# Optimization experiments

Measured on AMD Instinct MI355X. Metric: run time of the kernel, lower is better.

## Reference

```python
import jax, jax.numpy as jnp
import numpy as np

D = 1024   # model dim (hard-coded in ClsNet)
H = 16     # num_heads
HD = D // H
FF = 2048  # torch TransformerEncoderLayer default dim_feedforward
B, LX, LY = 8, 512, 512
EPS = 1e-5
NEG = -1e9


def setup_inputs() -> dict:
    key = jax.random.key(0)
    ks = jax.random.split(key, 16)
    s = 0.02
    inp = {
        "x": jax.random.normal(ks[0], (B, LX, D), jnp.float32),
        "y": jax.random.normal(ks[1], (B, LY, D), jnp.float32),
        "cls": jax.random.normal(ks[2], (D,), jnp.float32) * s,
        "sep": jax.random.normal(ks[3], (D,), jnp.float32) * s,
        "px": jax.random.normal(ks[4], (D,), jnp.float32) * s,
        "py": jax.random.normal(ks[5], (D,), jnp.float32) * s,
        "Wqkv": jax.random.normal(ks[6], (3 * D, D), jnp.float32) * s,
        "bqkv": jnp.zeros((3 * D,), jnp.float32),
        "Wo": jax.random.normal(ks[7], (D, D), jnp.float32) * s,
        "bo": jnp.zeros((D,), jnp.float32),
        "W1": jax.random.normal(ks[8], (FF, D), jnp.float32) * s,
        "b1": jnp.zeros((FF,), jnp.float32),
        "W2": jax.random.normal(ks[9], (D, FF), jnp.float32) * s,
        "b2": jnp.zeros((D,), jnp.float32),
        "ln1_g": jnp.ones((D,), jnp.float32),
        "ln1_b": jnp.zeros((D,), jnp.float32),
        "ln2_g": jnp.ones((D,), jnp.float32),
        "ln2_b": jnp.zeros((D,), jnp.float32),
        "x_len": jax.random.randint(ks[10], (B,), 1, LX + 1, jnp.int32),
        "y_len": jax.random.randint(ks[11], (B,), 1, LY + 1, jnp.int32),
    }
    return inp


def _merge(x, y, cls, sep, px, py, x_len, y_len):
    # Vectorized version of ClsNet.merge: [CLS] x_i+px ... [SEP] y_i+py ... [SEP] pad...
    Bn, Lx, Dd = x.shape
    Ly = y.shape[1]
    S = Lx + Ly + 3
    pos = jnp.arange(S)[None, :]            # [1,S]
    lx = x_len[:, None]                     # [B,1]
    ly = y_len[:, None]
    is_cls = pos == 0                       # [1,S]
    is_x = (pos >= 1) & (pos <= lx)         # [B,S]
    is_sep1 = pos == lx + 1
    is_y = (pos >= lx + 2) & (pos <= lx + ly + 1)
    is_sep2 = pos == lx + ly + 2
    xi = jnp.clip(pos - 1, 0, Lx - 1)       # [1,S]
    yi = jnp.clip(pos - lx - 2, 0, Ly - 1)  # [B,S]
    xg = jnp.take_along_axis(x, xi[:, :, None], axis=1)  # [B,S,D] (broadcast batch)
    yg = jnp.take_along_axis(y, yi[:, :, None], axis=1)  # [B,S,D]
    seq = (jnp.where(is_x[..., None], xg + px, 0.0)
           + jnp.where(is_y[..., None], yg + py, 0.0)
           + is_cls[..., None] * cls
           + (is_sep1 | is_sep2)[..., None] * sep)       # [B,S,D]
    mask = is_cls | is_x | is_sep1 | is_y | is_sep2      # [B,S] True = valid token
    return seq, mask


def _ln(h, g, b):
    m = jnp.mean(h, axis=-1, keepdims=True)
    v = jnp.mean(jnp.square(h - m), axis=-1, keepdims=True)
    return (h - m) * jax.lax.rsqrt(v + EPS) * g + b


def _encoder_layer(seq, mask, Wqkv, bqkv, Wo, bo, W1, b1, W2, b2, ln1_g, ln1_b, ln2_g, ln2_b):
    Bn, S, Dd = seq.shape
    qkv = seq @ Wqkv.T + bqkv                              # [B,S,3D]
    q, k, v = jnp.split(qkv, 3, axis=-1)
    q = q.reshape(Bn, S, H, HD)
    k = k.reshape(Bn, S, H, HD)
    v = v.reshape(Bn, S, H, HD)
    bias = jnp.where(mask, 0.0, NEG)[:, None, None, :]     # padded KEYS masked out
    scores = jnp.einsum("bqhd,bkhd->bhqk", q, k) / np.sqrt(HD) + bias
    attn = jax.nn.softmax(scores, axis=-1)
    o = jnp.einsum("bhqk,bkhd->bqhd", attn, v).reshape(Bn, S, Dd)
    o = o @ Wo.T + bo
    h = _ln(seq + o, ln1_g, ln1_b)                          # post-norm (torch default)
    f = jax.nn.relu(h @ W1.T + b1) @ W2.T + b2
    return _ln(h + f, ln2_g, ln2_b)


def reference(x, y, cls, sep, px, py, Wqkv, bqkv, Wo, bo, W1, b1, W2, b2,
              ln1_g, ln1_b, ln2_g, ln2_b, x_len, y_len):
    seq, mask = _merge(x, y, cls, sep, px, py, x_len, y_len)
    out = _encoder_layer(seq, mask, Wqkv, bqkv, Wo, bo, W1, b1, W2, b2,
                         ln1_g, ln1_b, ln2_g, ln2_b)
    # torch code returns a[0] of the seq-first tensor -> the CLS position for all batches
    return out[:, 0, :]
```

## Files before the change

### kernel.cpp

```cpp
#include <hip/hip_runtime.h>
#include <hip/hip_bf16.h>

#define D_ 1024
#define H_ 16
#define FF_ 2048
#define B_ 8
#define S_ 1027
#define MPAD_ 8320
#define PSTR_ 1056
#define EPS_ 1e-5f

typedef __hip_bfloat16 bf16;
typedef unsigned short u16;
typedef unsigned int u32;
typedef __attribute__((ext_vector_type(4))) float floatx4;
typedef __bf16 bf16x8 __attribute__((ext_vector_type(8)));

__device__ __forceinline__ float2 bfpair(u32 u) {
  union { u32 u; float f; } lo, hi;
  lo.u = u << 16; hi.u = u & 0xffff0000u;
  return make_float2(lo.f, hi.f);
}

__device__ __forceinline__ u32 f2bfbits(float f) {
  union { bf16 h; u16 u; } cv; cv.h = __float2bfloat16(f); return (u32)cv.u;
}

__device__ __forceinline__ float block_sum(float x, float* red) {
  const int t = threadIdx.x;
  __syncthreads();
  red[t] = x;
  __syncthreads();
  for (int s = 128; s > 0; s >>= 1) {
    if (t < s) red[t] += red[t + s];
    __syncthreads();
  }
  return red[0];
}

__device__ __forceinline__ float block_max(float x, float* red) {
  const int t = threadIdx.x;
  __syncthreads();
  red[t] = x;
  __syncthreads();
  for (int s = 128; s > 0; s >>= 1) {
    if (t < s) red[t] = fmaxf(red[t], red[t + s]);
    __syncthreads();
  }
  return red[0];
}

__global__ void __launch_bounds__(256) build_seq_kernel(
    const float* __restrict__ x, const float* __restrict__ y,
    const float* __restrict__ cls, const float* __restrict__ sep,
    const float* __restrict__ px, const float* __restrict__ py,
    const int* __restrict__ x_len, const int* __restrict__ y_len,
    bf16* __restrict__ seq) {
  const int m = blockIdx.x, t = threadIdx.x;
  const int b = m / S_;
  const int s = m - b * S_;
  if (b >= B_) return;
  const float* src = nullptr;
  const float* add = nullptr;
  const int lx = x_len[b], ly = y_len[b];
  if (s == 0) src = cls;
  else if (s <= lx) { src = x + ((size_t)b * 512 + (s - 1)) * D_; add = px; }
  else if (s == lx + 1) src = sep;
  else if (s <= lx + ly + 1) { src = y + ((size_t)b * 512 + (s - lx - 2)) * D_; add = py; }
  else if (s == lx + ly + 2) src = sep;
  if (!src) return;
  float4 sv = ((const float4*)src)[t];
  if (add) {
    float4 av = ((const float4*)add)[t];
    sv.x += av.x; sv.y += av.y; sv.z += av.z; sv.w += av.w;
  }
  uint2 o;
  o.x = f2bfbits(sv.x) | (f2bfbits(sv.y) << 16);
  o.y = f2bfbits(sv.z) | (f2bfbits(sv.w) << 16);
  ((uint2*)(seq + (size_t)m * D_))[t] = o;
}

__global__ void __launch_bounds__(256) qproj_kernel(
    const float* __restrict__ cls, const float* __restrict__ Wqkv,
    const float* __restrict__ bqkv, float* __restrict__ q0s) {
  __shared__ float cl[D_];
  const int t = threadIdx.x;
  *(float4*)&cl[t * 4] = ((const float4*)cls)[t];
  __syncthreads();
  const int w = t >> 6, l = t & 63;
  const int r = blockIdx.x * 4 + w;
  float acc = 0.f;
#pragma unroll
  for (int ch = 0; ch < 4; ++ch) {
    float4 wv = *(const float4*)(Wqkv + (size_t)r * D_ + ch * 256 + l * 4);
    const float* c4 = &cl[ch * 256 + l * 4];
    acc += wv.x * c4[0] + wv.y * c4[1] + wv.z * c4[2] + wv.w * c4[3];
  }
#pragma unroll
  for (int off = 32; off > 0; off >>= 1) acc += __shfl_down(acc, off, 64);
  if (l == 0) q0s[r] = (acc + bqkv[r]) * 0.125f;
}

__global__ void __launch_bounds__(256) rproj_kernel(
    const float* __restrict__ Wqkv, const float* __restrict__ q0s,
    u16* __restrict__ RT_hi, u16* __restrict__ RT_lo) {
  const int h = blockIdx.y, cc = blockIdx.x, t = threadIdx.x;
  __shared__ float qs[64];
  if (t < 64) qs[t] = q0s[h * 64 + t];
  __syncthreads();
  const int c = cc * 256 + t;
  const float* Wk = Wqkv + (size_t)(D_ + h * 64) * D_ + c;
  float acc = 0.f;
#pragma unroll 8
  for (int e = 0; e < 64; ++e) acc += Wk[(size_t)e * D_] * qs[e];
  const u32 hb = f2bfbits(acc);
  union { u32 u; float f; } hv; hv.u = hb << 16;
  RT_hi[h * D_ + c] = (u16)hb;
  RT_lo[h * D_ + c] = (u16)f2bfbits(acc - hv.f);
}

__global__ void __launch_bounds__(256) scores_kernel(
    const bf16* __restrict__ seq, const u16* __restrict__ RT_hi,
    const u16* __restrict__ RT_lo, const int* __restrict__ x_len,
    const int* __restrict__ y_len, float* __restrict__ S) {
  const int m0 = blockIdx.x * 64;
  bool valid = false;
#pragma unroll
  for (int b = 0; b < B_; ++b) {
    int rs = b * S_, re = rs + x_len[b] + y_len[b] + 3;
    if (m0 < re && m0 + 64 > rs) valid = true;
  }
  if (!valid) return;
  const int t = threadIdx.x;
  const int w = t >> 6, lane = t & 63, lane16 = lane & 15, quad = lane >> 4;
  const int row = m0 + w * 16 + lane16;
  const u16* arow = (const u16*)seq + (size_t)row * D_ + quad * 8;
  const u16* bh = RT_hi + lane16 * D_ + quad * 8;
  const u16* bl = RT_lo + lane16 * D_ + quad * 8;
  floatx4 acc = {};
#pragma unroll 4
  for (int kt = 0; kt < 32; ++kt) {
    bf16x8 a  = *(const bf16x8*)(arow + kt * 32);
    bf16x8 vh = *(const bf16x8*)(bh + kt * 32);
    bf16x8 vl = *(const bf16x8*)(bl + kt * 32);
    acc = __builtin_amdgcn_mfma_f32_16x16x32_bf16(a, vh, acc, 0, 0, 0);
    acc = __builtin_amdgcn_mfma_f32_16x16x32_bf16(a, vl, acc, 0, 0, 0);
  }
  *(floatx4*)&S[(size_t)lane16 * MPAD_ + m0 + w * 16 + quad * 4] = acc;
}

__global__ void __launch_bounds__(256) softmax_kernel(
    const float* __restrict__ S, const int* __restrict__ x_len,
    const int* __restrict__ y_len, u16* __restrict__ P) {
  const int h = blockIdx.x, b = blockIdx.y, t = threadIdx.x;
  const int n = x_len[b] + y_len[b] + 3;
  __shared__ float sc[PSTR_];
  __shared__ float red[256];
  const float* Sp = S + (size_t)h * MPAD_ + b * S_;
  float lmax = -3.0e38f;
  for (int k = t; k < n; k += 256) {
    float s = Sp[k];
    sc[k] = s;
    lmax = fmaxf(lmax, s);
  }
  const float gmax = block_max(lmax, red);
  float lsum = 0.f;
  for (int k = t; k < n; k += 256) {
    float p = __expf(sc[k] - gmax);
    sc[k] = p;
    lsum += p;
  }
  const float inv = 1.0f / block_sum(lsum, red);
  u16* Pp = P + (size_t)(h * 8 + b) * PSTR_;
  for (int k = t; k < PSTR_; k += 256)
    Pp[k] = (k < n) ? (u16)f2bfbits(sc[k] * inv) : (u16)0;
}

__global__ void __launch_bounds__(256) cbar_kernel(
    const bf16* __restrict__ seq, const u16* __restrict__ P,
    const int* __restrict__ x_len, const int* __restrict__ y_len,
    float* __restrict__ cbar) {
  const int ct = blockIdx.x, b = blockIdx.y, t = threadIdx.x;
  const int c0 = ct * 64;
  const int n = x_len[b] + y_len[b] + 3;
  const int nkt = (n + 31) >> 5;
  __shared__ u16 tile[32 * 68];
  const int w = t >> 6, lane = t & 63, lane16 = lane & 15, quad = lane >> 4;
  const int sk = t >> 3, scg = (t & 7) * 8;
  floatx4 acc = {};
  for (int kt = 0; kt < nkt; ++kt) {
    const int k0 = kt * 32;
    __syncthreads();
    uint4 v = make_uint4(0u, 0u, 0u, 0u);
    if (k0 + sk < n)
      v = *(const uint4*)((const u16*)seq + (size_t)(b * S_ + k0 + sk) * D_ + c0 + scg);
    *(uint2*)&tile[sk * 68 + scg]     = make_uint2(v.x, v.y);
    *(uint2*)&tile[sk * 68 + scg + 4] = make_uint2(v.z, v.w);
    __syncthreads();
    bf16x8 a = *(const bf16x8*)(P + (size_t)(lane16 * 8 + b) * PSTR_ + k0 + quad * 8);
    union { bf16x8 v; u16 u[8]; } bu;
#pragma unroll
    for (int j = 0; j < 8; ++j)
      bu.u[j] = tile[(quad * 8 + j) * 68 + w * 16 + lane16];
    acc = __builtin_amdgcn_mfma_f32_16x16x32_bf16(a, bu.v, acc, 0, 0, 0);
  }
#pragma unroll
  for (int r = 0; r < 4; ++r)
    cbar[(size_t)(b * 16 + quad * 4 + r) * D_ + c0 + w * 16 + lane16] = acc[r];
}

template <int K, int N, int BSTR, bool INBF, bool OUTBF, bool RELU, bool PERHEAD>
__global__ void __launch_bounds__(256) gemv8_kernel(
    const void* __restrict__ in_, const float* __restrict__ W,
    const float* __restrict__ bias, void* __restrict__ out_) {
  const int t = threadIdx.x;
  const int hoff = PERHEAD ? ((blockIdx.x * 4) >> 6) * D_ : 0;
  __shared__ u16 lsb[INBF ? 8 * K : 1];
  __shared__ float lsf[INBF ? 1 : 8 * K];
  if (INBF) {
    const u16* in = (const u16*)in_;
    const int per = 8 * K / (256 * 8);
#pragma unroll
    for (int i = 0; i < per; ++i) {
      int flat = (t + i * 256) * 8;
      int b = flat / K, k = flat % K;
      *(uint4*)&lsb[flat] = *(const uint4*)(in + (size_t)b * BSTR + hoff + k);
    }
  } else {
    const float* in = (const float*)in_;
    const int per = 8 * K / (256 * 4);
#pragma unroll
    for (int i = 0; i < per; ++i) {
      int flat = (t + i * 256) * 4;
      int b = flat / K, k = flat % K;
      *(float4*)&lsf[flat] = *(const float4*)(in + (size_t)b * BSTR + hoff + k);
    }
  }
  __syncthreads();
  const int w = t >> 6, l = t & 63;
  const int r = blockIdx.x * 4 + w;
  float acc[8] = {};
#pragma unroll
  for (int ch = 0; ch < K / 256; ++ch) {
    float4 wv = *(const float4*)(W + (size_t)r * K + ch * 256 + l * 4);
#pragma unroll
    for (int b = 0; b < 8; ++b) {
      float i0, i1, i2, i3;
      if (INBF) {
        uint2 u = *(const uint2*)&lsb[b * K + ch * 256 + l * 4];
        float2 p0 = bfpair(u.x), p1 = bfpair(u.y);
        i0 = p0.x; i1 = p0.y; i2 = p1.x; i3 = p1.y;
      } else {
        const float* p = &lsf[b * K + ch * 256 + l * 4];
        i0 = p[0]; i1 = p[1]; i2 = p[2]; i3 = p[3];
      }
      acc[b] += wv.x * i0 + wv.y * i1 + wv.z * i2 + wv.w * i3;
    }
  }
#pragma unroll
  for (int off = 32; off > 0; off >>= 1)
#pragma unroll
    for (int b = 0; b < 8; ++b) acc[b] += __shfl_down(acc[b], off, 64);
  if (l == 0) {
    const float bs = bias[r];
#pragma unroll
    for (int b = 0; b < 8; ++b) {
      float v = acc[b] + bs;
      if (RELU) v = fmaxf(v, 0.f);
      if (OUTBF) ((bf16*)out_)[(size_t)b * N + r] = __float2bfloat16(v);
      else       ((float*)out_)[(size_t)b * N + r] = v;
    }
  }
}

template <bool SECOND>
__global__ void __launch_bounds__(256) ln_kernel(
    const float* __restrict__ cls, const float* __restrict__ a,
    const float* __restrict__ bvec, const float* __restrict__ g,
    const float* __restrict__ be, float* __restrict__ out) {
  const int b = blockIdx.x, t = threadIdx.x;
  __shared__ float v[D_];
  __shared__ float red[256];
  for (int i = t; i < D_; i += 256) {
    float val;
    if (SECOND) val = a[b * D_ + i] + bvec[b * D_ + i];
    else        val = cls[i] + a[b * D_ + i];
    v[i] = val;
  }
  __syncthreads();
  float ls = 0.f;
  for (int i = t; i < D_; i += 256) ls += v[i];
  const float mean = block_sum(ls, red) * (1.f / D_);
  float lv = 0.f;
  for (int i = t; i < D_; i += 256) { float dk = v[i] - mean; lv += dk * dk; }
  const float var = block_sum(lv, red) * (1.f / D_);
  const float rs = rsqrtf(var + EPS_);
  for (int i = t; i < D_; i += 256)
    out[b * D_ + i] = (v[i] - mean) * rs * g[i] + be[i];
}

extern "C" void kernel_launch(void* const* d_in, const int* in_sizes, int n_in,
                              void* d_out, int out_size, void* d_ws, size_t ws_size,
                              hipStream_t stream) {
  (void)in_sizes; (void)n_in; (void)out_size; (void)ws_size;
  const float* x    = (const float*)d_in[0];
  const float* y    = (const float*)d_in[1];
  const float* cls  = (const float*)d_in[2];
  const float* sep  = (const float*)d_in[3];
  const float* px   = (const float*)d_in[4];
  const float* py   = (const float*)d_in[5];
  const float* Wqkv = (const float*)d_in[6];
  const float* bqkv = (const float*)d_in[7];
  const float* Wo   = (const float*)d_in[8];
  const float* bo   = (const float*)d_in[9];
  const float* W1   = (const float*)d_in[10];
  const float* b1   = (const float*)d_in[11];
  const float* W2   = (const float*)d_in[12];
  const float* b2   = (const float*)d_in[13];
  const float* g1   = (const float*)d_in[14];
  const float* be1  = (const float*)d_in[15];
  const float* g2   = (const float*)d_in[16];
  const float* be2  = (const float*)d_in[17];
  const int* xl     = (const int*)d_in[18];
  const int* yl     = (const int*)d_in[19];

  char* ws = (char*)d_ws;
  bf16*  seq   = (bf16*)(ws);
  float* q0s   = (float*)(ws + 17039360);
  u16*   RT_hi = (u16*)(ws + 17043456);
  u16*   RT_lo = (u16*)(ws + 17076224);
  float* S     = (float*)(ws + 17108992);
  u16*   P     = (u16*)(ws + 17641472);
  float* cbar  = (float*)(ws + 17911808);
  float* o0    = (float*)(ws + 18436096);
  float* att   = (float*)(ws + 18468864);
  float* h0    = (float*)(ws + 18501632);
  bf16*  f1    = (bf16*)(ws + 18534400);
  float* f2    = (float*)(ws + 18567168);

  build_seq_kernel<<<MPAD_, 256, 0, stream>>>(x, y, cls, sep, px, py, xl, yl, seq);
  qproj_kernel<<<256, 256, 0, stream>>>(cls, Wqkv, bqkv, q0s);
  rproj_kernel<<<dim3(4, 16), 256, 0, stream>>>(Wqkv, q0s, RT_hi, RT_lo);
  scores_kernel<<<130, 256, 0, stream>>>(seq, RT_hi, RT_lo, xl, yl, S);
  softmax_kernel<<<dim3(16, 8), 256, 0, stream>>>(S, xl, yl, P);
  cbar_kernel<<<dim3(16, 8), 256, 0, stream>>>(seq, P, xl, yl, cbar);
  gemv8_kernel<1024, 1024, 16384, false, false, false, true>
      <<<256, 256, 0, stream>>>(cbar, Wqkv + (size_t)2048 * 1024, bqkv + 2048, o0);
  gemv8_kernel<1024, 1024, 1024, false, false, false, false>
      <<<256, 256, 0, stream>>>(o0, Wo, bo, att);
  ln_kernel<false><<<B_, 256, 0, stream>>>(cls, att, nullptr, g1, be1, h0);
  gemv8_kernel<1024, 2048, 1024, false, true, true, false>
      <<<512, 256, 0, stream>>>(h0, W1, b1, f1);
  gemv8_kernel<2048, 1024, 2048, true, false, false, false>
      <<<256, 256, 0, stream>>>(f1, W2, b2, f2);
  ln_kernel<true><<<B_, 256, 0, stream>>>(nullptr, h0, f2, g2, be2, (float*)d_out);
}
```

Before: 195.3 us.

## Fuse the whole pipeline into one cooperative persistent kernel with grid syncs

```diff
diff --git a/kernel.cpp b/kernel.cpp
--- a/kernel.cpp
+++ b/kernel.cpp
@@ -1,14 +1,21 @@
 #include <hip/hip_runtime.h>
 #include <hip/hip_bf16.h>
+#include <hip/hip_cooperative_groups.h>
+
+namespace cg = cooperative_groups;
 
 #define D_ 1024
 #define H_ 16
 #define FF_ 2048
 #define B_ 8
 #define S_ 1027
+#define BS_ 8216
 #define MPAD_ 8320
 #define PSTR_ 1056
 #define EPS_ 1e-5f
+#define MAXGRID_ 512
+#define NTILE_ 130
+#define SPLIT_KT_ 17
 
 typedef __hip_bfloat16 bf16;
 typedef unsigned short u16;
@@ -24,6 +31,376 @@
 
 __device__ __forceinline__ u32 f2bfbits(float f) {
   union { bf16 h; u16 u; } cv; cv.h = __float2bfloat16(f); return (u32)cv.u;
+}
+
+__device__ __forceinline__ float blk_sum(float x, float* red) {
+#pragma unroll
+  for (int off = 32; off > 0; off >>= 1) x += __shfl_down(x, off, 64);
+  __syncthreads();
+  if ((threadIdx.x & 63) == 0) red[threadIdx.x >> 6] = x;
+  __syncthreads();
+  return red[0] + red[1] + red[2] + red[3];
+}
+
+__device__ __forceinline__ float blk_max(float x, float* red) {
+#pragma unroll
+  for (int off = 32; off > 0; off >>= 1) x = fmaxf(x, __shfl_down(x, off, 64));
+  __syncthreads();
+  if ((threadIdx.x & 63) == 0) red[threadIdx.x >> 6] = x;
+  __syncthreads();
+  return fmaxf(fmaxf(red[0], red[1]), fmaxf(red[2], red[3]));
+}
+
+struct KP {
+  const float *x, *y, *cls, *sep, *px, *py;
+  const float *Wqkv, *bqkv, *Wo, *bo, *W1, *b1, *W2, *b2;
+  const float *g1, *be1, *g2, *be2;
+  const int *xl, *yl;
+  bf16* seq; float* q0s; u16* RT_hi; u16* RT_lo; float* S; u16* P;
+  float* cbar; float* cbar2; float* o0; float* att; float* h0;
+  bf16* f1; float* f2; float* out;
+};
+
+__global__ void __launch_bounds__(256, 2) mega_kernel(KP p) {
+  __shared__ __align__(16) char smem_[33792];
+  cg::grid_group grid = cg::this_grid();
+  const int t = threadIdx.x;
+  const int bid = blockIdx.x;
+  const int G = gridDim.x;
+
+  for (int m = bid; m < BS_; m += G) {
+    const int b = m / S_;
+    const int s = m - b * S_;
+    const int lx = p.xl[b], ly = p.yl[b];
+    const float* src = nullptr;
+    const float* add = nullptr;
+    if (s == 0) src = p.cls;
+    else if (s <= lx) { src = p.x + ((size_t)b * 512 + (s - 1)) * D_; add = p.px; }
+    else if (s == lx + 1) src = p.sep;
+    else if (s <= lx + ly + 1) { src = p.y + ((size_t)b * 512 + (s - lx - 2)) * D_; add = p.py; }
+    else if (s == lx + ly + 2) src = p.sep;
+    if (src) {
+      float4 sv = ((const float4*)src)[t];
+      if (add) {
+        float4 av = ((const float4*)add)[t];
+        sv.x += av.x; sv.y += av.y; sv.z += av.z; sv.w += av.w;
+      }
+      uint2 o;
+      o.x = f2bfbits(sv.x) | (f2bfbits(sv.y) << 16);
+      o.y = f2bfbits(sv.z) | (f2bfbits(sv.w) << 16);
+      ((uint2*)(p.seq + (size_t)m * D_))[t] = o;
+    }
+  }
+  for (int wk = bid; wk < 256; wk += G) {
+    float* cl = (float*)smem_;
+    *(float4*)&cl[t * 4] = ((const float4*)p.cls)[t];
+    __syncthreads();
+    const int w = t >> 6, l = t & 63;
+    const int r = wk * 4 + w;
+    float acc = 0.f;
+#pragma unroll
+    for (int ch = 0; ch < 4; ++ch) {
+      float4 wv = *(const float4*)(p.Wqkv + (size_t)r * D_ + ch * 256 + l * 4);
+      const float* c4 = &cl[ch * 256 + l * 4];
+      acc += wv.x * c4[0] + wv.y * c4[1] + wv.z * c4[2] + wv.w * c4[3];
+    }
+#pragma unroll
+    for (int off = 32; off > 0; off >>= 1) acc += __shfl_down(acc, off, 64);
+    if (l == 0) p.q0s[r] = (acc + p.bqkv[r]) * 0.125f;
+    __syncthreads();
+  }
+  grid.sync();
+
+  for (int wk = bid; wk < 512; wk += G) {
+    float* red = (float*)smem_;
+    const int h = wk >> 5, chunk = wk & 31;
+    const int c = chunk * 32 + (t & 31);
+    const int es = t >> 5;
+    const float* Wk = p.Wqkv + (size_t)(D_ + h * 64) * D_ + c;
+    const float* q = p.q0s + h * 64 + es * 8;
+    float acc = 0.f;
+#pragma unroll
+    for (int i = 0; i < 8; ++i)
+      acc += Wk[(size_t)(es * 8 + i) * D_] * q[i];
+    red[t] = acc;
+    __syncthreads();
+    if (t < 32) {
+      float a = red[t];
+#pragma unroll
+      for (int i = 1; i < 8; ++i) a += red[i * 32 + t];
+      const u32 hb = f2bfbits(a);
+      union { u32 u; float f; } hv; hv.u = hb << 16;
+      p.RT_hi[h * D_ + c] = (u16)hb;
+      p.RT_lo[h * D_ + c] = (u16)f2bfbits(a - hv.f);
+    }
+    __syncthreads();
+  }
+  grid.sync();
+
+  for (int wk = bid; wk < NTILE_; wk += G) {
+    const int m0 = wk * 64;
+    bool valid = false;
+#pragma unroll
+    for (int b = 0; b < B_; ++b) {
+      int rs = b * S_, re = rs + p.xl[b] + p.yl[b] + 3;
+      if (m0 < re && m0 + 64 > rs) valid = true;
+    }
+    if (!valid) continue;
+    const int w = t >> 6, lane = t & 63, lane16 = lane & 15, quad = lane >> 4;
+    const int row = m0 + w * 16 + lane16;
+    const u16* arow = (const u16*)p.seq + (size_t)row * D_ + quad * 8;
+    const u16* bh = p.RT_hi + lane16 * D_ + quad * 8;
+    const u16* bl = p.RT_lo + lane16 * D_ + quad * 8;
+    floatx4 acc = {};
+#pragma unroll 4
+    for (int kt = 0; kt < 32; ++kt) {
+      bf16x8 a  = *(const bf16x8*)(arow + kt * 32);
+      bf16x8 vh = *(const bf16x8*)(bh + kt * 32);
+      bf16x8 vl = *(const bf16x8*)(bl + kt * 32);
+      acc = __builtin_amdgcn_mfma_f32_16x16x32_bf16(a, vh, acc, 0, 0, 0);
+      acc = __builtin_amdgcn_mfma_f32_16x16x32_bf16(a, vl, acc, 0, 0, 0);
+    }
+    *(floatx4*)&p.S[(size_t)lane16 * MPAD_ + m0 + w * 16 + quad * 4] = acc;
+  }
+  grid.sync();
+
+  for (int wk = bid; wk < 128; wk += G) {
+    const int h = wk >> 3, b = wk & 7;
+    const int n = p.xl[b] + p.yl[b] + 3;
+    float* sc = (float*)smem_;
+    float* red = (float*)(smem_ + PSTR_ * 4);
+    const float* Sp = p.S + (size_t)h * MPAD_ + b * S_;
+    float lmax = -3.0e38f;
+    for (int k = t; k < n; k += 256) {
+      float s = Sp[k];
+      sc[k] = s;
+      lmax = fmaxf(lmax, s);
+    }
+    const float gmax = blk_max(lmax, red);
+    float lsum = 0.f;
+    for (int k = t; k < n; k += 256) {
+      float pr = __expf(sc[k] - gmax);
+      sc[k] = pr;
+      lsum += pr;
+    }
+    const float inv = 1.0f / blk_sum(lsum, red);
+    u16* Pp = p.P + (size_t)(h * 8 + b) * PSTR_;
+    for (int k = t; k < PSTR_; k += 256)
+      Pp[k] = (k < n) ? (u16)f2bfbits(sc[k] * inv) : (u16)0;
+    __syncthreads();
+  }
+  grid.sync();
+
+  for (int wk = bid; wk < 256; wk += G) {
+    const int ct = wk & 15, b = (wk >> 4) & 7, half = wk >> 7;
+    const int c0 = ct * 64;
+    const int n = p.xl[b] + p.yl[b] + 3;
+    const int nkt = (n + 31) >> 5;
+    const int kt0 = half ? SPLIT_KT_ : 0;
+    const int kt1 = half ? nkt : (nkt < SPLIT_KT_ ? nkt : SPLIT_KT_);
+    u16* tile = (u16*)smem_;
+    const int w = t >> 6, lane = t & 63, lane16 = lane & 15, quad = lane >> 4;
+    const int sk = t >> 3, scg = (t & 7) * 8;
+    floatx4 acc = {};
+    uint4 v = make_uint4(0u, 0u, 0u, 0u);
+    if (kt0 < kt1 && kt0 * 32 + sk < n)
+      v = *(const uint4*)((const u16*)p.seq + (size_t)((size_t)b * S_ + kt0 * 32 + sk) * D_ + c0 + scg);
+    for (int kt = kt0; kt < kt1; ++kt) {
+      u16* tb = tile + (kt & 1) * (32 * 68);
+      *(uint2*)&tb[sk * 68 + scg]     = make_uint2(v.x, v.y);
+      *(uint2*)&tb[sk * 68 + scg + 4] = make_uint2(v.z, v.w);
+      v = make_uint4(0u, 0u, 0u, 0u);
+      if (kt + 1 < kt1 && (kt + 1) * 32 + sk < n)
+        v = *(const uint4*)((const u16*)p.seq + (size_t)((size_t)b * S_ + (kt + 1) * 32 + sk) * D_ + c0 + scg);
+      __syncthreads();
+      bf16x8 a = *(const bf16x8*)(p.P + (size_t)(lane16 * 8 + b) * PSTR_ + kt * 32 + quad * 8);
+      union { bf16x8 v8; u16 u[8]; } bu;
+#pragma unroll
+      for (int j = 0; j < 8; ++j)
+        bu.u[j] = tb[(quad * 8 + j) * 68 + w * 16 + lane16];
+      acc = __builtin_amdgcn_mfma_f32_16x16x32_bf16(a, bu.v8, acc, 0, 0, 0);
+    }
+    float* dst = half ? p.cbar2 : p.cbar;
+#pragma unroll
+    for (int r = 0; r < 4; ++r)
+      dst[(size_t)(b * 16 + quad * 4 + r) * D_ + c0 + w * 16 + lane16] = acc[r];
+    __syncthreads();
+  }
+  grid.sync();
+
+  for (int wk = bid; wk < 256; wk += G) {
+    float* lsf = (float*)smem_;
+    const int hoff = ((wk * 4) >> 6) * D_;
+#pragma unroll
+    for (int i = 0; i < 8; ++i) {
+      int flat = (t + i * 256) * 4;
+      int b = flat >> 10, k = flat & 1023;
+      size_t off = (size_t)b * 16384 + hoff + k;
+      float4 a0 = *(const float4*)(p.cbar + off);
+      float4 a1 = *(const float4*)(p.cbar2 + off);
+      a0.x += a1.x; a0.y += a1.y; a0.z += a1.z; a0.w += a1.w;
+      *(float4*)&lsf[flat] = a0;
+    }
+    __syncthreads();
+    const int w = t >> 6, l = t & 63;
+    const int r = wk * 4 + w;
+    const float* W = p.Wqkv + (size_t)2048 * 1024;
+    float acc[8] = {};
+#pragma unroll
+    for (int ch = 0; ch < 4; ++ch) {
+      float4 wv = *(const float4*)(W + (size_t)r * D_ + ch * 256 + l * 4);
+#pragma unroll
+      for (int b = 0; b < 8; ++b) {
+        const float* pp = &lsf[b * D_ + ch * 256 + l * 4];
+        acc[b] += wv.x * pp[0] + wv.y * pp[1] + wv.z * pp[2] + wv.w * pp[3];
+      }
+    }
+#pragma unroll
+    for (int off = 32; off > 0; off >>= 1)
+#pragma unroll
+      for (int b = 0; b < 8; ++b) acc[b] += __shfl_down(acc[b], off, 64);
+    if (l == 0) {
+      const float bs = p.bqkv[2048 + r];
+#pragma unroll
+      for (int b = 0; b < 8; ++b) p.o0[(size_t)b * D_ + r] = acc[b] + bs;
+    }
+    __syncthreads();
+  }
+  grid.sync();
+
+  for (int wk = bid; wk < 256; wk += G) {
+    float* lsf = (float*)smem_;
+#pragma unroll
+    for (int i = 0; i < 8; ++i) {
+      int flat = (t + i * 256) * 4;
+      *(float4*)&lsf[flat] = *(const float4*)(p.o0 + flat);
+    }
+    __syncthreads();
+    const int w = t >> 6, l = t & 63;
+    const int r = wk * 4 + w;
+    float acc[8] = {};
+#pragma unroll
+    for (int ch = 0; ch < 4; ++ch) {
+      float4 wv = *(const float4*)(p.Wo + (size_t)r * D_ + ch * 256 + l * 4);
+#pragma unroll
+      for (int b = 0; b < 8; ++b) {
+        const float* pp = &lsf[b * D_ + ch * 256 + l * 4];
+        acc[b] += wv.x * pp[0] + wv.y * pp[1] + wv.z * pp[2] + wv.w * pp[3];
+      }
+    }
+#pragma unroll
+    for (int off = 32; off > 0; off >>= 1)
+#pragma unroll
+      for (int b = 0; b < 8; ++b) acc[b] += __shfl_down(acc[b], off, 64);
+    if (l == 0) {
+      const float bs = p.bo[r];
+#pragma unroll
+      for (int b = 0; b < 8; ++b) p.att[(size_t)b * D_ + r] = acc[b] + bs;
+    }
+    __syncthreads();
+  }
+  grid.sync();
+
+  for (int wk = bid; wk < 8; wk += G) {
+    float* v = (float*)smem_;
+    float* red = (float*)(smem_ + D_ * 4);
+    for (int i = t; i < D_; i += 256) v[i] = p.cls[i] + p.att[wk * D_ + i];
+    float ls = 0.f;
+    for (int i = t; i < D_; i += 256) ls += v[i];
+    const float mean = blk_sum(ls, red) * (1.f / D_);
+    float lv = 0.f;
+    for (int i = t; i < D_; i += 256) { float dk = v[i] - mean; lv += dk * dk; }
+    const float var = blk_sum(lv, red) * (1.f / D_);
+    const float rs = rsqrtf(var + EPS_);
+    for (int i = t; i < D_; i += 256)
+      p.h0[wk * D_ + i] = (v[i] - mean) * rs * p.g1[i] + p.be1[i];
+    __syncthreads();
+  }
+  grid.sync();
+
+  for (int wk = bid; wk < 512; wk += G) {
+    float* lsf = (float*)smem_;
+#pragma unroll
+    for (int i = 0; i < 8; ++i) {
+      int flat = (t + i * 256) * 4;
+      *(float4*)&lsf[flat] = *(const float4*)(p.h0 + flat);
+    }
+    __syncthreads();
+    const int w = t >> 6, l = t & 63;
+    const int r = wk * 4 + w;
+    float acc[8] = {};
+#pragma unroll
+    for (int ch = 0; ch < 4; ++ch) {
+      float4 wv = *(const float4*)(p.W1 + (size_t)r * D_ + ch * 256 + l * 4);
+#pragma unroll
+      for (int b = 0; b < 8; ++b) {
+        const float* pp = &lsf[b * D_ + ch * 256 + l * 4];
+        acc[b] += wv.x * pp[0] + wv.y * pp[1] + wv.z * pp[2] + wv.w * pp[3];
+      }
+    }
+#pragma unroll
+    for (int off = 32; off > 0; off >>= 1)
+#pragma unroll
+      for (int b = 0; b < 8; ++b) acc[b] += __shfl_down(acc[b], off, 64);
+    if (l == 0) {
+      const float bs = p.b1[r];
+#pragma unroll
+      for (int b = 0; b < 8; ++b)
+        p.f1[(size_t)b * FF_ + r] = __float2bfloat16(fmaxf(acc[b] + bs, 0.f));
+    }
+    __syncthreads();
+  }
+  grid.sync();
+
+  for (int wk = bid; wk < 256; wk += G) {
+    u16* lsb = (u16*)smem_;
+#pragma unroll
+    for (int i = 0; i < 8; ++i) {
+      int flat = (t + i * 256) * 8;
+      *(uint4*)&lsb[flat] = *(const uint4*)((const u16*)p.f1 + flat);
+    }
+    __syncthreads();
+    const int w = t >> 6, l = t & 63;
+    const int r = wk * 4 + w;
+    float acc[8] = {};
+#pragma unroll
+    for (int ch = 0; ch < 8; ++ch) {
+      float4 wv = *(const float4*)(p.W2 + (size_t)r * FF_ + ch * 256 + l * 4);
+#pragma unroll
+      for (int b = 0; b < 8; ++b) {
+        uint2 u = *(const uint2*)&lsb[b * FF_ + ch * 256 + l * 4];
+        float2 p0 = bfpair(u.x), p1 = bfpair(u.y);
+        acc[b] += wv.x * p0.x + wv.y * p0.y + wv.z * p1.x + wv.w * p1.y;
+      }
+    }
+#pragma unroll
+    for (int off = 32; off > 0; off >>= 1)
+#pragma unroll
+      for (int b = 0; b < 8; ++b) acc[b] += __shfl_down(acc[b], off, 64);
+    if (l == 0) {
+      const float bs = p.b2[r];
+#pragma unroll
+      for (int b = 0; b < 8; ++b) p.f2[(size_t)b * D_ + r] = acc[b] + bs;
+    }
+    __syncthreads();
+  }
+  grid.sync();
+
+  for (int wk = bid; wk < 8; wk += G) {
+    float* v = (float*)smem_;
+    float* red = (float*)(smem_ + D_ * 4);
+    for (int i = t; i < D_; i += 256) v[i] = p.h0[wk * D_ + i] + p.f2[wk * D_ + i];
+    float ls = 0.f;
+    for (int i = t; i < D_; i += 256) ls += v[i];
+    const float mean = blk_sum(ls, red) * (1.f / D_);
+    float lv = 0.f;
+    for (int i = t; i < D_; i += 256) { float dk = v[i] - mean; lv += dk * dk; }
+    const float var = blk_sum(lv, red) * (1.f / D_);
+    const float rs = rsqrtf(var + EPS_);
+    for (int i = t; i < D_; i += 256)
+      p.out[wk * D_ + i] = (v[i] - mean) * rs * p.g2[i] + p.be2[i];
+    __syncthreads();
+  }
 }
 
 __device__ __forceinline__ float block_sum(float x, float* red) {
@@ -332,26 +709,60 @@
   float* S     = (float*)(ws + 17108992);
   u16*   P     = (u16*)(ws + 17641472);
   float* cbar  = (float*)(ws + 17911808);
-  float* o0    = (float*)(ws + 18436096);
-  float* att   = (float*)(ws + 18468864);
-  float* h0    = (float*)(ws + 18501632);
-  bf16*  f1    = (bf16*)(ws + 18534400);
-  float* f2    = (float*)(ws + 18567168);
-
-  build_seq_kernel<<<MPAD_, 256, 0, stream>>>(x, y, cls, sep, px, py, xl, yl, seq);
-  qproj_kernel<<<256, 256, 0, stream>>>(cls, Wqkv, bqkv, q0s);
-  rproj_kernel<<<dim3(4, 16), 256, 0, stream>>>(Wqkv, q0s, RT_hi, RT_lo);
-  scores_kernel<<<130, 256, 0, stream>>>(seq, RT_hi, RT_lo, xl, yl, S);
-  softmax_kernel<<<dim3(16, 8), 256, 0, stream>>>(S, xl, yl, P);
-  cbar_kernel<<<dim3(16, 8), 256, 0, stream>>>(seq, P, xl, yl, cbar);
-  gemv8_kernel<1024, 1024, 16384, false, false, false, true>
-      <<<256, 256, 0, stream>>>(cbar, Wqkv + (size_t)2048 * 1024, bqkv + 2048, o0);
-  gemv8_kernel<1024, 1024, 1024, false, false, false, false>
-      <<<256, 256, 0, stream>>>(o0, Wo, bo, att);
-  ln_kernel<false><<<B_, 256, 0, stream>>>(cls, att, nullptr, g1, be1, h0);
-  gemv8_kernel<1024, 2048, 1024, false, true, true, false>
-      <<<512, 256, 0, stream>>>(h0, W1, b1, f1);
-  gemv8_kernel<2048, 1024, 2048, true, false, false, false>
-      <<<256, 256, 0, stream>>>(f1, W2, b2, f2);
-  ln_kernel<true><<<B_, 256, 0, stream>>>(nullptr, h0, f2, g2, be2, (float*)d_out);
-}
+  float* cbar2 = (float*)(ws + 18436096);
+  float* o0    = (float*)(ws + 18960384);
+  float* att   = (float*)(ws + 18993152);
+  float* h0    = (float*)(ws + 19025920);
+  bf16*  f1    = (bf16*)(ws + 19058688);
+  float* f2    = (float*)(ws + 19091456);
+
+  KP kp;
+  kp.x = x; kp.y = y; kp.cls = cls; kp.sep = sep; kp.px = px; kp.py = py;
+  kp.Wqkv = Wqkv; kp.bqkv = bqkv; kp.Wo = Wo; kp.bo = bo;
+  kp.W1 = W1; kp.b1 = b1; kp.W2 = W2; kp.b2 = b2;
+  kp.g1 = g1; kp.be1 = be1; kp.g2 = g2; kp.be2 = be2;
+  kp.xl = xl; kp.yl = yl;
+  kp.seq = seq; kp.q0s = q0s; kp.RT_hi = RT_hi; kp.RT_lo = RT_lo;
+  kp.S = S; kp.P = P; kp.cbar = cbar; kp.cbar2 = cbar2;
+  kp.o0 = o0; kp.att = att; kp.h0 = h0; kp.f1 = f1; kp.f2 = f2;
+  kp.out = (float*)d_out;
+
+  static int coop_grid = -2;
+  if (coop_grid == -2) {
+    int nb = 0;
+    if (hipOccupancyMaxActiveBlocksPerMultiprocessor(&nb, mega_kernel, 256, 0) ==
+            hipSuccess && nb > 0) {
+      long g = (long)nb * 256;
+      coop_grid = (int)(g < MAXGRID_ ? g : MAXGRID_);
+    } else {
+      coop_grid = -1;
+    }
+  }
+
+  bool ok = false;
+  if (coop_grid > 0) {
+    void* args[] = { (void*)&kp };
+    ok = hipLaunchCooperativeKernel(mega_kernel, dim3(coop_grid), dim3(256),
+                                    args, 0u, stream) == hipSuccess;
+    if (!ok) (void)hipGetLastError();
+  }
+
+  if (!ok) {
+    build_seq_kernel<<<MPAD_, 256, 0, stream>>>(x, y, cls, sep, px, py, xl, yl, seq);
+    qproj_kernel<<<256, 256, 0, stream>>>(cls, Wqkv, bqkv, q0s);
+    rproj_kernel<<<dim3(4, 16), 256, 0, stream>>>(Wqkv, q0s, RT_hi, RT_lo);
+    scores_kernel<<<130, 256, 0, stream>>>(seq, RT_hi, RT_lo, xl, yl, S);
+    softmax_kernel<<<dim3(16, 8), 256, 0, stream>>>(S, xl, yl, P);
+    cbar_kernel<<<dim3(16, 8), 256, 0, stream>>>(seq, P, xl, yl, cbar);
+    gemv8_kernel<1024, 1024, 16384, false, false, false, true>
+        <<<256, 256, 0, stream>>>(cbar, Wqkv + (size_t)2048 * 1024, bqkv + 2048, o0);
+    gemv8_kernel<1024, 1024, 1024, false, false, false, false>
+        <<<256, 256, 0, stream>>>(o0, Wo, bo, att);
+    ln_kernel<false><<<B_, 256, 0, stream>>>(cls, att, nullptr, g1, be1, h0);
+    gemv8_kernel<1024, 2048, 1024, false, true, true, false>
+        <<<512, 256, 0, stream>>>(h0, W1, b1, f1);
+    gemv8_kernel<2048, 1024, 2048, true, false, false, false>
+        <<<256, 256, 0, stream>>>(f1, W2, b2, f2);
+    ln_kernel<true><<<B_, 256, 0, stream>>>(nullptr, h0, f2, g2, be2, (float*)d_out);
+  }
+}
```

Result: slower. 491.9 us (+151.9%).
